# Optimization experiments

Hardware: AMD Instinct MI355X
Metric: run time of the kernel (lower is better)

Reference implementation:

```python
import jax, jax.numpy as jnp
import numpy as np

N_NODES = 200000
N_DIM = 64
N_EDGES = 6400000
N_LAYERS = 3


def setup_inputs() -> dict:
    key = jax.random.key(0)
    k1, k2, k3, k4 = jax.random.split(key, 4)
    emb = jax.random.normal(k1, (N_NODES, N_DIM), dtype=jnp.float32) * 0.1
    edge_vals = jax.random.uniform(k2, (N_EDGES,), dtype=jnp.float32)
    rows = jax.random.randint(k3, (N_EDGES,), 0, N_NODES, dtype=jnp.int32)
    cols = jax.random.randint(k4, (N_EDGES,), 0, N_NODES, dtype=jnp.int32)
    return {"emb": emb, "edge_vals": edge_vals, "rows": rows, "cols": cols}


def _spmm(edge_vals, rows, cols, x):
    # y[r] = sum_{e: rows[e]==r} edge_vals[e] * x[cols[e]]
    msgs = edge_vals[:, None] * x[cols]          # [E, D] gather + scale
    return jax.ops.segment_sum(msgs, rows, num_segments=N_NODES)


def reference(emb, edge_vals, rows, cols):
    # LightGCN forward: dropout=0 so graph is used as-is; propagate n_layers
    # times and mean over the (n_layers+1) layer embeddings.
    acc = emb
    h = emb
    for _ in range(N_LAYERS):
        h = _spmm(edge_vals, rows, cols, h)
        acc = acc + h
    return acc / (N_LAYERS + 1)
```

## Files before the change

### kernel.cpp

```cpp
#include <hip/hip_runtime.h>

#define N_NODES 200000
#define N_DIM   64
#define N_EDGES 6400000
#define NBK     3125
#define NSB     250
#define EPB     (N_EDGES/NSB)
#define ROWSORT_CAP 4096

__global__ __launch_bounds__(256) void k_hist(const int* __restrict__ rows,
                                              int* __restrict__ mat) {
    __shared__ int h[NBK];
    int t = threadIdx.x;
    for (int i = t; i < NBK; i += 256) h[i] = 0;
    __syncthreads();
    int start = blockIdx.x * EPB;
    for (int j = t; j < EPB; j += 256) {
        int r = rows[start + j];
        atomicAdd(&h[r >> 6], 1);
    }
    __syncthreads();
    int* m = mat + blockIdx.x * NBK;
    for (int i = t; i < NBK; i += 256) m[i] = h[i];
}

__global__ __launch_bounds__(256) void k_tot(const int* __restrict__ mat,
                                             int* __restrict__ tot) {
    int b = blockIdx.x * 256 + threadIdx.x;
    if (b >= NBK) return;
    int s = 0;
    for (int blk = 0; blk < NSB; ++blk) s += mat[blk * NBK + b];
    tot[b] = s;
}

__global__ __launch_bounds__(256) void k_scanbase(const int* __restrict__ tot,
                                                  int* __restrict__ base) {
    __shared__ int sm[256];
    int t = threadIdx.x;
    const int C = 13;
    int c0 = t * C;
    int loc[C];
    int s = 0;
#pragma unroll
    for (int i = 0; i < C; ++i) {
        int b = c0 + i;
        loc[i] = (b < NBK) ? tot[b] : 0;
        s += loc[i];
    }
    sm[t] = s;
    __syncthreads();
    for (int off = 1; off < 256; off <<= 1) {
        int x = (t >= off) ? sm[t - off] : 0;
        __syncthreads();
        sm[t] += x;
        __syncthreads();
    }
    int run = (t == 0) ? 0 : sm[t - 1];
#pragma unroll
    for (int i = 0; i < C; ++i) {
        int b = c0 + i;
        if (b < NBK) base[b] = run;
        run += loc[i];
    }
    if (t == 255) base[NBK] = run;
}

__global__ __launch_bounds__(256) void k_rebase(int* __restrict__ mat,
                                                const int* __restrict__ base) {
    int b = blockIdx.x * 256 + threadIdx.x;
    if (b >= NBK) return;
    int run = base[b];
    for (int blk = 0; blk < NSB; ++blk) {
        int v = mat[blk * NBK + b];
        mat[blk * NBK + b] = run;
        run += v;
    }
}

__global__ __launch_bounds__(256) void k_scatter(const int* __restrict__ rows,
                                                 const int* __restrict__ cols,
                                                 const float* __restrict__ vals,
                                                 const int* __restrict__ mat,
                                                 int2* __restrict__ slots) {
    __shared__ int cur[NBK];
    int t = threadIdx.x;
    const int* m = mat + blockIdx.x * NBK;
    for (int i = t; i < NBK; i += 256) cur[i] = m[i];
    __syncthreads();
    int start = blockIdx.x * EPB;
    for (int j = t; j < EPB; j += 256) {
        int e = start + j;
        int r = rows[e];
        int pos = atomicAdd(&cur[r >> 6], 1);
        slots[pos] = make_int2(((r & 63) << 18) | cols[e], __float_as_int(vals[e]));
    }
}

__global__ __launch_bounds__(256) void k_rowsort(const int* __restrict__ base,
                                                 int2* __restrict__ slots,
                                                 int2* __restrict__ spill,
                                                 int* __restrict__ offsets) {
    __shared__ int2 buf[ROWSORT_CAP];
    __shared__ int cnt[64], pos[64], cursor[64];
    int t = threadIdx.x, b = blockIdx.x;
    int s0 = base[b], s1 = base[b + 1], n = s1 - s0;
    if (t < 64) cnt[t] = 0;
    __syncthreads();
    bool lds = (n <= ROWSORT_CAP);
    if (lds) {
        for (int i = t; i < n; i += 256) {
            int2 v = slots[s0 + i];
            buf[i] = v;
            atomicAdd(&cnt[((unsigned)v.x) >> 18], 1);
        }
    } else {
        for (int i = t; i < n; i += 256) {
            int2 v = slots[s0 + i];
            spill[s0 + i] = v;
            atomicAdd(&cnt[((unsigned)v.x) >> 18], 1);
        }
        __threadfence();
    }
    __syncthreads();
    if (t == 0) {
        int run = 0;
        for (int r = 0; r < 64; ++r) { int c = cnt[r]; pos[r] = run; cursor[r] = run; run += c; }
    }
    __syncthreads();
    if (t < 64) offsets[(b << 6) + t] = s0 + pos[t];
    if (t == 64 && b == NBK - 1) offsets[N_NODES] = s1;
    if (lds) {
        for (int i = t; i < n; i += 256) {
            int2 v = buf[i];
            int p = atomicAdd(&cursor[((unsigned)v.x) >> 18], 1);
            slots[s0 + p] = make_int2(v.x & 0x3FFFF, v.y);
        }
    } else {
        for (int i = t; i < n; i += 256) {
            int2 v = spill[s0 + i];
            int p = atomicAdd(&cursor[((unsigned)v.x) >> 18], 1);
            slots[s0 + p] = make_int2(v.x & 0x3FFFF, v.y);
        }
    }
}

template <int MODE>
__global__ __launch_bounds__(256) void spmm(const int* __restrict__ offsets,
                                            const int2* __restrict__ slots,
                                            const float* __restrict__ x,
                                            float* __restrict__ y,
                                            const float* __restrict__ emb,
                                            float* __restrict__ out) {
    int t    = threadIdx.x;
    int r    = blockIdx.x * 16 + (t >> 4);
    int lane = t & 15;
    int j0 = offsets[r], j1 = offsets[r + 1];

    float4 acc = make_float4(0.f, 0.f, 0.f, 0.f);
    int j = j0;
    for (; j + 4 <= j1; j += 4) {
        int2 e0 = slots[j], e1 = slots[j + 1], e2 = slots[j + 2], e3 = slots[j + 3];
        const float4 x0 = *reinterpret_cast<const float4*>(x + (e0.x << 6) + (lane << 2));
        const float4 x1 = *reinterpret_cast<const float4*>(x + (e1.x << 6) + (lane << 2));
        const float4 x2 = *reinterpret_cast<const float4*>(x + (e2.x << 6) + (lane << 2));
        const float4 x3 = *reinterpret_cast<const float4*>(x + (e3.x << 6) + (lane << 2));
        float v0 = __int_as_float(e0.y), v1 = __int_as_float(e1.y);
        float v2 = __int_as_float(e2.y), v3 = __int_as_float(e3.y);
        acc.x = fmaf(v0, x0.x, acc.x); acc.y = fmaf(v0, x0.y, acc.y);
        acc.z = fmaf(v0, x0.z, acc.z); acc.w = fmaf(v0, x0.w, acc.w);
        acc.x = fmaf(v1, x1.x, acc.x); acc.y = fmaf(v1, x1.y, acc.y);
        acc.z = fmaf(v1, x1.z, acc.z); acc.w = fmaf(v1, x1.w, acc.w);
        acc.x = fmaf(v2, x2.x, acc.x); acc.y = fmaf(v2, x2.y, acc.y);
        acc.z = fmaf(v2, x2.z, acc.z); acc.w = fmaf(v2, x2.w, acc.w);
        acc.x = fmaf(v3, x3.x, acc.x); acc.y = fmaf(v3, x3.y, acc.y);
        acc.z = fmaf(v3, x3.z, acc.z); acc.w = fmaf(v3, x3.w, acc.w);
    }
    for (; j < j1; ++j) {
        int2 e = slots[j];
        const float4 xr = *reinterpret_cast<const float4*>(x + (e.x << 6) + (lane << 2));
        float v = __int_as_float(e.y);
        acc.x = fmaf(v, xr.x, acc.x); acc.y = fmaf(v, xr.y, acc.y);
        acc.z = fmaf(v, xr.z, acc.z); acc.w = fmaf(v, xr.w, acc.w);
    }

    int o = (r << 6) + (lane << 2);
    if (MODE == 0) {
        float4 e = *reinterpret_cast<const float4*>(emb + o);
        *reinterpret_cast<float4*>(y + o) = acc;
        *reinterpret_cast<float4*>(out + o) =
            make_float4(e.x + acc.x, e.y + acc.y, e.z + acc.z, e.w + acc.w);
    } else if (MODE == 1) {
        float4 a = *reinterpret_cast<const float4*>(out + o);
        *reinterpret_cast<float4*>(y + o) = acc;
        *reinterpret_cast<float4*>(out + o) =
            make_float4(a.x + acc.x, a.y + acc.y, a.z + acc.z, a.w + acc.w);
    } else {
        float4 a = *reinterpret_cast<const float4*>(out + o);
        *reinterpret_cast<float4*>(out + o) =
            make_float4((a.x + acc.x) * 0.25f, (a.y + acc.y) * 0.25f,
                        (a.z + acc.z) * 0.25f, (a.w + acc.w) * 0.25f);
    }
}

extern "C" void kernel_launch(void* const* d_in, const int* in_sizes, int n_in,
                              void* d_out, int out_size, void* d_ws, size_t ws_size,
                              hipStream_t stream) {
    const float* emb  = (const float*)d_in[0];
    const float* vals = (const float*)d_in[1];
    const int*   rows = (const int*)d_in[2];
    const int*   cols = (const int*)d_in[3];
    float*       out  = (float*)d_out;
    char*        ws   = (char*)d_ws;

    const size_t OFF_SLOTS  = 0;
    const size_t OFF_MAT    = 51200000;
    const size_t OFF_TOT    = 54325248;
    const size_t OFF_BASE   = 54337792;
    const size_t OFF_ROWOFF = 54350336;
    const size_t OFF_BUFA   = 55150592;
    const size_t OFF_BUFB   = 106350592;

    int2*  slots  = (int2*)(ws + OFF_SLOTS);
    int*   mat    = (int*)(ws + OFF_MAT);
    int*   tot    = (int*)(ws + OFF_TOT);
    int*   base   = (int*)(ws + OFF_BASE);
    int*   rowoff = (int*)(ws + OFF_ROWOFF);
    float* bufA   = (float*)(ws + OFF_BUFA);
    float* bufB   = (float*)(ws + OFF_BUFB);

    k_hist    <<<NSB,  256, 0, stream>>>(rows, mat);
    k_tot     <<<13,   256, 0, stream>>>(mat, tot);
    k_scanbase<<<1,    256, 0, stream>>>(tot, base);
    k_rebase  <<<13,   256, 0, stream>>>(mat, base);
    k_scatter <<<NSB,  256, 0, stream>>>(rows, cols, vals, mat, slots);
    k_rowsort <<<NBK,  256, 0, stream>>>(base, slots, (int2*)bufB, rowoff);

    spmm<0><<<N_NODES / 16, 256, 0, stream>>>(rowoff, slots, emb,  bufA, emb, out);
    spmm<1><<<N_NODES / 16, 256, 0, stream>>>(rowoff, slots, bufA, bufB, nullptr, out);
    spmm<2><<<N_NODES / 16, 256, 0, stream>>>(rowoff, slots, bufB, nullptr, nullptr, out);
}
```

Measured before the change: 1.132 ms.

## Sort edges by column tile within rows and sweep tiles across row groups

The row-sort kernel now orders each row's edges by column tile as well (16 tiles of 12500 columns) and writes per-row, per-tile counts as bytes. The SpMM kernel gives each 16-lane group 13 rows and walks the tiles in order across all of them, so the gathered x rows for a block fall within one column range at a time. The aim is better L2/MALL locality for the random gathers. The cost is a larger sort histogram and scan, 13 float4 accumulators per thread with extra register pressure, and lower per-row memory-level parallelism from the 2-way unroll. The per-row-tile counts are stored as bytes, which assumes no row has more than 255 edges in one tile.

Result: slower. 1.660 ms (+46.7%).

```diff
diff --git a/kernel.cpp b/kernel.cpp
--- a/kernel.cpp
+++ b/kernel.cpp
@@ -7,6 +7,11 @@
 #define NSB     250
 #define EPB     (N_EDGES/NSB)
 #define ROWSORT_CAP 4096
+#define T_TILES 16
+#define TILE_DIV 12500
+#define RPB 208
+#define RPG 13
+#define SPMM_BLOCKS ((N_NODES + RPB - 1) / RPB)
 
 __global__ __launch_bounds__(256) void k_hist(const int* __restrict__ rows,
                                               int* __restrict__ mat) {
@@ -99,106 +104,165 @@
 __global__ __launch_bounds__(256) void k_rowsort(const int* __restrict__ base,
                                                  int2* __restrict__ slots,
                                                  int2* __restrict__ spill,
-                                                 int* __restrict__ offsets) {
+                                                 int* __restrict__ rowoff,
+                                                 unsigned char* __restrict__ cnt8) {
     __shared__ int2 buf[ROWSORT_CAP];
-    __shared__ int cnt[64], pos[64], cursor[64];
+    __shared__ int cnt2[1024], pos2[1024], cur2[1024];
+    __shared__ int sm[256];
     int t = threadIdx.x, b = blockIdx.x;
     int s0 = base[b], s1 = base[b + 1], n = s1 - s0;
-    if (t < 64) cnt[t] = 0;
+    for (int i = t; i < 1024; i += 256) cnt2[i] = 0;
     __syncthreads();
     bool lds = (n <= ROWSORT_CAP);
     if (lds) {
         for (int i = t; i < n; i += 256) {
             int2 v = slots[s0 + i];
             buf[i] = v;
-            atomicAdd(&cnt[((unsigned)v.x) >> 18], 1);
+            int col = v.x & 0x3FFFF;
+            int key = ((((unsigned)v.x) >> 18) << 4) | (unsigned)(col / TILE_DIV);
+            atomicAdd(&cnt2[key], 1);
         }
     } else {
         for (int i = t; i < n; i += 256) {
             int2 v = slots[s0 + i];
             spill[s0 + i] = v;
-            atomicAdd(&cnt[((unsigned)v.x) >> 18], 1);
+            int col = v.x & 0x3FFFF;
+            int key = ((((unsigned)v.x) >> 18) << 4) | (unsigned)(col / TILE_DIV);
+            atomicAdd(&cnt2[key], 1);
         }
         __threadfence();
     }
     __syncthreads();
-    if (t == 0) {
-        int run = 0;
-        for (int r = 0; r < 64; ++r) { int c = cnt[r]; pos[r] = run; cursor[r] = run; run += c; }
-    }
-    __syncthreads();
-    if (t < 64) offsets[(b << 6) + t] = s0 + pos[t];
-    if (t == 64 && b == NBK - 1) offsets[N_NODES] = s1;
+    int b4 = t << 2;
+    int l0 = cnt2[b4], l1 = cnt2[b4 + 1], l2 = cnt2[b4 + 2], l3 = cnt2[b4 + 3];
+    sm[t] = l0 + l1 + l2 + l3;
+    __syncthreads();
+    for (int off = 1; off < 256; off <<= 1) {
+        int xv = (t >= off) ? sm[t - off] : 0;
+        __syncthreads();
+        sm[t] += xv;
+        __syncthreads();
+    }
+    int run = (t == 0) ? 0 : sm[t - 1];
+    pos2[b4] = run;           cur2[b4] = run;
+    pos2[b4 + 1] = run + l0;  cur2[b4 + 1] = run + l0;
+    pos2[b4 + 2] = run + l0 + l1;       cur2[b4 + 2] = run + l0 + l1;
+    pos2[b4 + 3] = run + l0 + l1 + l2;  cur2[b4 + 3] = run + l0 + l1 + l2;
+    __syncthreads();
+    if (t < 64) {
+        int gr = (b << 6) + t;
+        rowoff[gr] = s0 + pos2[t << 4];
+#pragma unroll
+        for (int tt = 0; tt < T_TILES; ++tt)
+            cnt8[tt * N_NODES + gr] = (unsigned char)cnt2[(t << 4) + tt];
+    }
+    __syncthreads();
     if (lds) {
         for (int i = t; i < n; i += 256) {
             int2 v = buf[i];
-            int p = atomicAdd(&cursor[((unsigned)v.x) >> 18], 1);
-            slots[s0 + p] = make_int2(v.x & 0x3FFFF, v.y);
+            int col = v.x & 0x3FFFF;
+            int key = ((((unsigned)v.x) >> 18) << 4) | (unsigned)(col / TILE_DIV);
+            int p = atomicAdd(&cur2[key], 1);
+            slots[s0 + p] = make_int2(col, v.y);
         }
     } else {
         for (int i = t; i < n; i += 256) {
             int2 v = spill[s0 + i];
-            int p = atomicAdd(&cursor[((unsigned)v.x) >> 18], 1);
-            slots[s0 + p] = make_int2(v.x & 0x3FFFF, v.y);
+            int col = v.x & 0x3FFFF;
+            int key = ((((unsigned)v.x) >> 18) << 4) | (unsigned)(col / TILE_DIV);
+            int p = atomicAdd(&cur2[key], 1);
+            slots[s0 + p] = make_int2(col, v.y);
         }
     }
 }
 
 template <int MODE>
-__global__ __launch_bounds__(256) void spmm(const int* __restrict__ offsets,
-                                            const int2* __restrict__ slots,
+__global__ __launch_bounds__(256) void spmm(const int* __restrict__ rowoff,
+                                            const unsigned char* __restrict__ cnt8,
+                                            const long long* __restrict__ slots,
                                             const float* __restrict__ x,
                                             float* __restrict__ y,
                                             const float* __restrict__ emb,
                                             float* __restrict__ out) {
     int t    = threadIdx.x;
-    int r    = blockIdx.x * 16 + (t >> 4);
+    int g    = t >> 4;
     int lane = t & 15;
-    int j0 = offsets[r], j1 = offsets[r + 1];
-
-    float4 acc = make_float4(0.f, 0.f, 0.f, 0.f);
-    int j = j0;
-    for (; j + 4 <= j1; j += 4) {
-        int2 e0 = slots[j], e1 = slots[j + 1], e2 = slots[j + 2], e3 = slots[j + 3];
-        const float4 x0 = *reinterpret_cast<const float4*>(x + (e0.x << 6) + (lane << 2));
-        const float4 x1 = *reinterpret_cast<const float4*>(x + (e1.x << 6) + (lane << 2));
-        const float4 x2 = *reinterpret_cast<const float4*>(x + (e2.x << 6) + (lane << 2));
-        const float4 x3 = *reinterpret_cast<const float4*>(x + (e3.x << 6) + (lane << 2));
-        float v0 = __int_as_float(e0.y), v1 = __int_as_float(e1.y);
-        float v2 = __int_as_float(e2.y), v3 = __int_as_float(e3.y);
-        acc.x = fmaf(v0, x0.x, acc.x); acc.y = fmaf(v0, x0.y, acc.y);
-        acc.z = fmaf(v0, x0.z, acc.z); acc.w = fmaf(v0, x0.w, acc.w);
-        acc.x = fmaf(v1, x1.x, acc.x); acc.y = fmaf(v1, x1.y, acc.y);
-        acc.z = fmaf(v1, x1.z, acc.z); acc.w = fmaf(v1, x1.w, acc.w);
-        acc.x = fmaf(v2, x2.x, acc.x); acc.y = fmaf(v2, x2.y, acc.y);
-        acc.z = fmaf(v2, x2.z, acc.z); acc.w = fmaf(v2, x2.w, acc.w);
-        acc.x = fmaf(v3, x3.x, acc.x); acc.y = fmaf(v3, x3.y, acc.y);
-        acc.z = fmaf(v3, x3.z, acc.z); acc.w = fmaf(v3, x3.w, acc.w);
-    }
-    for (; j < j1; ++j) {
-        int2 e = slots[j];
-        const float4 xr = *reinterpret_cast<const float4*>(x + (e.x << 6) + (lane << 2));
-        float v = __int_as_float(e.y);
-        acc.x = fmaf(v, xr.x, acc.x); acc.y = fmaf(v, xr.y, acc.y);
-        acc.z = fmaf(v, xr.z, acc.z); acc.w = fmaf(v, xr.w, acc.w);
-    }
-
-    int o = (r << 6) + (lane << 2);
-    if (MODE == 0) {
-        float4 e = *reinterpret_cast<const float4*>(emb + o);
-        *reinterpret_cast<float4*>(y + o) = acc;
-        *reinterpret_cast<float4*>(out + o) =
-            make_float4(e.x + acc.x, e.y + acc.y, e.z + acc.z, e.w + acc.w);
-    } else if (MODE == 1) {
-        float4 a = *reinterpret_cast<const float4*>(out + o);
-        *reinterpret_cast<float4*>(y + o) = acc;
-        *reinterpret_cast<float4*>(out + o) =
-            make_float4(a.x + acc.x, a.y + acc.y, a.z + acc.z, a.w + acc.w);
-    } else {
-        float4 a = *reinterpret_cast<const float4*>(out + o);
-        *reinterpret_cast<float4*>(out + o) =
-            make_float4((a.x + acc.x) * 0.25f, (a.y + acc.y) * 0.25f,
-                        (a.z + acc.z) * 0.25f, (a.w + acc.w) * 0.25f);
+    int r0   = blockIdx.x * RPB + g * RPG;
+
+    float4 acc[RPG];
+    int cur[RPG];
+#pragma unroll
+    for (int i = 0; i < RPG; ++i) {
+        acc[i] = make_float4(0.f, 0.f, 0.f, 0.f);
+        int r = r0 + i;
+        cur[i] = (r < N_NODES) ? rowoff[r] : 0;
+    }
+
+    for (int tt = 0; tt < T_TILES; ++tt) {
+        const unsigned char* cp = cnt8 + tt * N_NODES;
+#pragma unroll
+        for (int i = 0; i < RPG; ++i) {
+            int r = r0 + i;
+            if (r < N_NODES) {
+                int c  = cp[r];
+                int j  = cur[i], je = j + c;
+                cur[i] = je;
+                for (; j + 2 <= je; j += 2) {
+                    unsigned long long e0 = *(const unsigned long long*)&slots[j];
+                    unsigned long long e1 = *(const unsigned long long*)&slots[j + 1];
+                    const float4 x0 = *reinterpret_cast<const float4*>(
+                        x + (((int)(e0 & 0x3FFFFu)) << 6) + (lane << 2));
+                    const float4 x1 = *reinterpret_cast<const float4*>(
+                        x + (((int)(e1 & 0x3FFFFu)) << 6) + (lane << 2));
+                    float v0 = __int_as_float((int)(e0 >> 32));
+                    float v1 = __int_as_float((int)(e1 >> 32));
+                    acc[i].x = fmaf(v0, x0.x, acc[i].x);
+                    acc[i].y = fmaf(v0, x0.y, acc[i].y);
+                    acc[i].z = fmaf(v0, x0.z, acc[i].z);
+                    acc[i].w = fmaf(v0, x0.w, acc[i].w);
+                    acc[i].x = fmaf(v1, x1.x, acc[i].x);
+                    acc[i].y = fmaf(v1, x1.y, acc[i].y);
+                    acc[i].z = fmaf(v1, x1.z, acc[i].z);
+                    acc[i].w = fmaf(v1, x1.w, acc[i].w);
+                }
+                if (j < je) {
+                    unsigned long long e0 = *(const unsigned long long*)&slots[j];
+                    const float4 x0 = *reinterpret_cast<const float4*>(
+                        x + (((int)(e0 & 0x3FFFFu)) << 6) + (lane << 2));
+                    float v0 = __int_as_float((int)(e0 >> 32));
+                    acc[i].x = fmaf(v0, x0.x, acc[i].x);
+                    acc[i].y = fmaf(v0, x0.y, acc[i].y);
+                    acc[i].z = fmaf(v0, x0.z, acc[i].z);
+                    acc[i].w = fmaf(v0, x0.w, acc[i].w);
+                }
+            }
+        }
+    }
+
+#pragma unroll
+    for (int i = 0; i < RPG; ++i) {
+        int r = r0 + i;
+        if (r < N_NODES) {
+            int o = (r << 6) + (lane << 2);
+            if (MODE == 0) {
+                float4 e = *reinterpret_cast<const float4*>(emb + o);
+                *reinterpret_cast<float4*>(y + o) = acc[i];
+                *reinterpret_cast<float4*>(out + o) =
+                    make_float4(e.x + acc[i].x, e.y + acc[i].y,
+                                e.z + acc[i].z, e.w + acc[i].w);
+            } else if (MODE == 1) {
+                float4 a = *reinterpret_cast<const float4*>(out + o);
+                *reinterpret_cast<float4*>(y + o) = acc[i];
+                *reinterpret_cast<float4*>(out + o) =
+                    make_float4(a.x + acc[i].x, a.y + acc[i].y,
+                                a.z + acc[i].z, a.w + acc[i].w);
+            } else {
+                float4 a = *reinterpret_cast<const float4*>(out + o);
+                *reinterpret_cast<float4*>(out + o) =
+                    make_float4((a.x + acc[i].x) * 0.25f, (a.y + acc[i].y) * 0.25f,
+                                (a.z + acc[i].z) * 0.25f, (a.w + acc[i].w) * 0.25f);
+            }
+        }
     }
 }
 
@@ -213,29 +277,33 @@
     char*        ws   = (char*)d_ws;
 
     const size_t OFF_SLOTS  = 0;
-    const size_t OFF_MAT    = 51200000;
-    const size_t OFF_TOT    = 54325248;
-    const size_t OFF_BASE   = 54337792;
-    const size_t OFF_ROWOFF = 54350336;
-    const size_t OFF_BUFA   = 55150592;
-    const size_t OFF_BUFB   = 106350592;
-
-    int2*  slots  = (int2*)(ws + OFF_SLOTS);
-    int*   mat    = (int*)(ws + OFF_MAT);
-    int*   tot    = (int*)(ws + OFF_TOT);
-    int*   base   = (int*)(ws + OFF_BASE);
-    int*   rowoff = (int*)(ws + OFF_ROWOFF);
-    float* bufA   = (float*)(ws + OFF_BUFA);
-    float* bufB   = (float*)(ws + OFF_BUFB);
-
-    k_hist    <<<NSB,  256, 0, stream>>>(rows, mat);
-    k_tot     <<<13,   256, 0, stream>>>(mat, tot);
-    k_scanbase<<<1,    256, 0, stream>>>(tot, base);
-    k_rebase  <<<13,   256, 0, stream>>>(mat, base);
-    k_scatter <<<NSB,  256, 0, stream>>>(rows, cols, vals, mat, slots);
-    k_rowsort <<<NBK,  256, 0, stream>>>(base, slots, (int2*)bufB, rowoff);
-
-    spmm<0><<<N_NODES / 16, 256, 0, stream>>>(rowoff, slots, emb,  bufA, emb, out);
-    spmm<1><<<N_NODES / 16, 256, 0, stream>>>(rowoff, slots, bufA, bufB, nullptr, out);
-    spmm<2><<<N_NODES / 16, 256, 0, stream>>>(rowoff, slots, bufB, nullptr, nullptr, out);
-}
+    const size_t OFF_CNT8   = 51200000;
+    const size_t OFF_TOT    = 54400000;
+    const size_t OFF_BASE   = 54450000;
+    const size_t OFF_ROWOFF = 54500016;
+    const size_t OFF_BUFA   = 55300016;
+    const size_t OFF_BUFB   = 106500016;
+
+    int2*          slots  = (int2*)(ws + OFF_SLOTS);
+    unsigned char* cnt8   = (unsigned char*)(ws + OFF_CNT8);
+    int*           tot    = (int*)(ws + OFF_TOT);
+    int*           base   = (int*)(ws + OFF_BASE);
+    int*           rowoff = (int*)(ws + OFF_ROWOFF);
+    float*         bufA   = (float*)(ws + OFF_BUFA);
+    float*         bufB   = (float*)(ws + OFF_BUFB);
+    int*           mat    = (int*)(ws + OFF_BUFA);
+
+    k_hist    <<<NSB, 256, 0, stream>>>(rows, mat);
+    k_tot     <<<13,  256, 0, stream>>>(mat, tot);
+    k_scanbase<<<1,   256, 0, stream>>>(tot, base);
+    k_rebase  <<<13,  256, 0, stream>>>(mat, base);
+    k_scatter <<<NSB, 256, 0, stream>>>(rows, cols, vals, mat, slots);
+    k_rowsort <<<NBK, 256, 0, stream>>>(base, slots, (int2*)bufB, rowoff, cnt8);
+
+    spmm<0><<<SPMM_BLOCKS, 256, 0, stream>>>(rowoff, cnt8, (const long long*)slots,
+                                             emb,  bufA, emb, out);
+    spmm<1><<<SPMM_BLOCKS, 256, 0, stream>>>(rowoff, cnt8, (const long long*)slots,
+                                             bufA, bufB, nullptr, out);
+    spmm<2><<<SPMM_BLOCKS, 256, 0, stream>>>(rowoff, cnt8, (const long long*)slots,
+                                             bufB, nullptr, nullptr, out);
+}
```
